# Kernel tuning notes

Hardware: AMD Instinct MI355X
Metric: run time of the kernel (lower is better)

The kernel has to match this reference:

```python
import jax, jax.numpy as jnp
import numpy as np

D_MODEL = 1024
N_HEADS = 16
HEAD_DIM = D_MODEL // N_HEADS


def setup_inputs() -> dict:
    key = jax.random.key(0)
    ks = jax.random.split(key, 9)
    s = 1.0 / np.sqrt(D_MODEL)
    mk = lambda k: jax.random.uniform(k, (D_MODEL, D_MODEL), jnp.float32, -s, s)
    mb = lambda k: jax.random.uniform(k, (D_MODEL,), jnp.float32, -s, s)
    return {
        "x": jax.random.normal(ks[0], (2, 2048, D_MODEL), jnp.float32),
        "Wq": mk(ks[1]), "bq": mb(ks[2]),
        "Wk": mk(ks[3]), "bk": mb(ks[4]),
        "Wv": mk(ks[5]), "bv": mb(ks[6]),
        "Wo": mk(ks[7]), "bo": mb(ks[8]),
    }


def _split_heads(t, B, S):
    # [B,S,D] -> [B,H,S,hd]
    return t.reshape(B, S, N_HEADS, HEAD_DIM).transpose(0, 2, 1, 3)


def reference(x, Wq, bq, Wk, bk, Wv, bv, Wo, bo):
    B, S, _ = x.shape
    # torch Linear: y = x @ W.T + b  (W stored [out, in])
    Q = _split_heads(x @ Wq.T + bq, B, S)
    K = _split_heads(x @ Wk.T + bk, B, S)
    V = _split_heads(x @ Wv.T + bv, B, S)
    scores = jnp.einsum("bhsd,bhtd->bhst", Q, K) / np.sqrt(HEAD_DIM).astype(np.float32)
    attn = jax.nn.softmax(scores, axis=-1)
    out = jnp.einsum("bhst,bhtd->bhsd", attn, V)
    out = out.transpose(0, 2, 1, 3).reshape(B, S, D_MODEL)
    return out @ Wo.T + bo
```

## Files before the change

kernel.cpp:

```cpp
#include <hip/hip_runtime.h>
#include <math.h>

#define D_MODEL 1024
#define NH 16
#define HD 64
#define SEQ 2048
#define NB 2
#define BSROWS (NB * SEQ)
#define NT (SEQ / 64)

typedef __attribute__((ext_vector_type(8)))  short short8;
typedef __attribute__((ext_vector_type(4)))  float f32x4;
typedef __attribute__((ext_vector_type(16))) float f32x16;

__device__ __forceinline__ ushort bf16rne(float f) {
    union { float f; uint32_t u; } v; v.f = f;
    return (ushort)((v.u + 0x7FFFu + ((v.u >> 16) & 1u)) >> 16);
}

__device__ __forceinline__ float hw_exp2(float x) {
    float r;
    asm("v_exp_f32 %0, %1" : "=v"(r) : "v"(x));
    return r;
}

__device__ __forceinline__ void permswap(uint32_t& a, uint32_t& b) {
    asm("v_permlane32_swap_b32 %0, %1" : "+v"(a), "+v"(b));
}

__device__ __forceinline__ void gl_lds16(const void* g, void* l) {
    __builtin_amdgcn_global_load_lds(
        reinterpret_cast<const uint32_t __attribute__((address_space(1)))*>(
            reinterpret_cast<uintptr_t>(g)),
        reinterpret_cast<uint32_t __attribute__((address_space(3)))*>(
            reinterpret_cast<uintptr_t>(l)),
        16, 0, 0);
}

__global__ __launch_bounds__(256) void convert_all(const float* __restrict__ x,
                                                   const float* __restrict__ w0,
                                                   const float* __restrict__ w1,
                                                   const float* __restrict__ w2,
                                                   const float* __restrict__ w3,
                                                   ushort* __restrict__ xb,
                                                   ushort* __restrict__ qkv,
                                                   ushort* __restrict__ wo) {
    const int which = blockIdx.y;
    const float* src;
    ushort* dst;
    int i;
    if (which < 4) {
        src = (which == 0) ? w0 : (which == 1) ? w1 : (which == 2) ? w2 : w3;
        dst = (which < 3) ? (qkv + (size_t)which * D_MODEL * D_MODEL) : wo;
        i   = blockIdx.x * 256 + threadIdx.x;
    } else {
        src = x;
        dst = xb;
        i   = ((which - 4) * 512 + blockIdx.x) * 256 + threadIdx.x;
    }
    const float4 a = ((const float4*)src)[2 * i];
    const float4 b = ((const float4*)src)[2 * i + 1];
    union { ushort u[8]; uint4 v; } r;
    r.u[0] = bf16rne(a.x); r.u[1] = bf16rne(a.y); r.u[2] = bf16rne(a.z); r.u[3] = bf16rne(a.w);
    r.u[4] = bf16rne(b.x); r.u[5] = bf16rne(b.y); r.u[6] = bf16rne(b.z); r.u[7] = bf16rne(b.w);
    ((uint4*)dst)[i] = r.v;
}

template <int BN, int MODE>
__global__ __launch_bounds__(256) void gemm_mfma(const ushort* __restrict__ A,
                                                 const ushort* __restrict__ B,
                                                 const float* __restrict__ b0,
                                                 const float* __restrict__ b1,
                                                 const float* __restrict__ b2,
                                                 void* __restrict__ o0v,
                                                 void* __restrict__ o1v,
                                                 void* __restrict__ o2v) {
    constexpr int BM = 128, BK = 32;
    constexpr int WN = (BN == 128) ? 64 : 32;
    constexpr int NM = 4;
    constexpr int NN = WN / 16;

    __shared__ ushort As[BM * BK];
    __shared__ ushort Bs[BN * BK];

    const int tid = threadIdx.x;
    const int w   = tid >> 6;
    const int l   = tid & 63;
    const int i0  = blockIdx.x * BM;
    const int n0  = blockIdx.y * BN;

    const int wr = (w >> 1) * 64;
    const int wc = (w & 1) * WN;

    const int srow = l >> 2;
    const int scol = (l & 3) * 8;
    const ushort* ga = A + (size_t)(i0 + w * 32 + srow) * D_MODEL + scol;
    const ushort* gb = B + (size_t)(n0 + w * (BN / 4) + srow) * D_MODEL + scol;
    ushort* lA = &As[(w * 32) * BK];
    ushort* lB = &Bs[(w * (BN / 4)) * BK];

    f32x4 acc[NM][NN];
#pragma unroll
    for (int m = 0; m < NM; ++m)
#pragma unroll
        for (int n = 0; n < NN; ++n) acc[m][n] = (f32x4){0.f, 0.f, 0.f, 0.f};

    const int fr = l & 15;
    const int kc = (l >> 4) * 8;

    for (int k0 = 0; k0 < D_MODEL; k0 += BK) {
        __syncthreads();
        gl_lds16(ga, lA);
        gl_lds16(ga + 16 * D_MODEL, lA + 16 * BK);
        gl_lds16(gb, lB);
        if (BN == 128) gl_lds16(gb + 16 * D_MODEL, lB + 16 * BK);
        ga += BK; gb += BK;
        __syncthreads();

        short8 af[NM], bfr[NN];
#pragma unroll
        for (int m = 0; m < NM; ++m)
            af[m] = *(const short8*)&As[(wr + m * 16 + fr) * BK + kc];
#pragma unroll
        for (int n = 0; n < NN; ++n)
            bfr[n] = *(const short8*)&Bs[(wc + n * 16 + fr) * BK + kc];
#pragma unroll
        for (int m = 0; m < NM; ++m)
#pragma unroll
            for (int n = 0; n < NN; ++n)
                acc[m][n] = __builtin_amdgcn_mfma_f32_16x16x32_bf16(af[m], bfr[n], acc[m][n], 0, 0, 0);
    }

    const int rr = (l >> 4) * 4;

    if (MODE == 1) {
        float* out = (float*)o0v;
#pragma unroll
        for (int n = 0; n < NN; ++n) {
            const int j = n0 + wc + n * 16 + fr;
            const float bj = b0[j];
#pragma unroll
            for (int m = 0; m < NM; ++m) {
                const int row = i0 + wr + m * 16 + rr;
#pragma unroll
                for (int r = 0; r < 4; ++r)
                    out[(size_t)(row + r) * D_MODEL + j] = acc[m][n][r] + bj;
            }
        }
    } else {
        const int p = n0 >> 10;
        const float* bias = (p == 0) ? b0 : (p == 1) ? b1 : b2;
        const float scl = (p == 0) ? 0.18033688011112042f : 1.0f;
#pragma unroll
        for (int n = 0; n < NN; ++n) {
            const int j = n0 + wc + n * 16 + fr;
            const int f = j & 1023;
            const float bj = bias[f];
            const int h = f >> 6, d = f & 63;
#pragma unroll
            for (int m = 0; m < NM; ++m) {
                const int row = i0 + wr + m * 16 + rr;
                const int bb = row >> 11;
                const int s0 = row & (SEQ - 1);
                if (p < 2) {
                    ushort* dst = (ushort*)(p == 0 ? o0v : o1v);
#pragma unroll
                    for (int r = 0; r < 4; ++r)
                        dst[(((size_t)bb * NH + h) * SEQ + (s0 + r)) * HD + d] =
                            bf16rne((acc[m][n][r] + bj) * scl);
                } else {
                    ushort4 pk;
                    pk.x = bf16rne(acc[m][n][0] + bj);
                    pk.y = bf16rne(acc[m][n][1] + bj);
                    pk.z = bf16rne(acc[m][n][2] + bj);
                    pk.w = bf16rne(acc[m][n][3] + bj);
                    *(ushort4*)&((ushort*)o2v)[(((size_t)bb * NH + h) * HD + d) * SEQ + s0] = pk;
                }
            }
        }
    }
}

__global__ __launch_bounds__(256) void attn_mfma9(const ushort* __restrict__ Q,
                                                  const ushort* __restrict__ K,
                                                  const ushort* __restrict__ Vt,
                                                  ushort* __restrict__ Aout) {
    __shared__ ushort KsB[2 * 4096];
    __shared__ ushort VtsB[2 * 4096];

    const int tid = threadIdx.x;
    const int w   = tid >> 6;
    const int l   = tid & 63;
    const int lq  = l & 31;
    const int hi  = l >> 5;
    const int id  = blockIdx.x;
    const int qt  = id >> 5;
    const int b   = (id >> 4) & 1;
    const int h   = id & 15;
    const size_t bh = (size_t)b * NH + h;

    const ushort* Qg = Q  + (bh * SEQ + (size_t)qt * 128 + w * 32 + lq) * HD;
    const ushort* Kg = K  + bh * SEQ * HD;
    const ushort* Vg = Vt + bh * HD * SEQ;

    short8 qf[4];
#pragma unroll
    for (int dk = 0; dk < 4; ++dk)
        qf[dk] = *(const short8*)&Qg[dk * 16 + hi * 8];

    int srow[2], scol[2], ssw[2];
#pragma unroll
    for (int j = 0; j < 2; ++j) {
        const int idx = tid + j * 256;
        srow[j] = idx >> 3;
        scol[j] = (idx & 7) * 8;
        ssw[j]  = scol[j] ^ ((srow[j] & 7) << 3);
    }

    uint4 kreg[2], vreg[2];
#pragma unroll
    for (int j = 0; j < 2; ++j) {
        kreg[j] = *(const uint4*)&Kg[(size_t)srow[j] * HD + scol[j]];
        vreg[j] = *(const uint4*)&Vg[(size_t)srow[j] * SEQ + scol[j]];
    }
#pragma unroll
    for (int j = 0; j < 2; ++j) {
        *(uint4*)&KsB [srow[j] * 64 + ssw[j]] = kreg[j];
        *(uint4*)&VtsB[srow[j] * 64 + ssw[j]] = vreg[j];
    }
    __syncthreads();

    f32x16 oa0a, oa0b, oa1a, oa1b;
#pragma unroll
    for (int r = 0; r < 16; ++r) { oa0a[r] = 0.f; oa0b[r] = 0.f; oa1a[r] = 0.f; oa1b[r] = 0.f; }
    float m = -3.0e38f, lsum = 0.f;

    for (int kt = 0; kt < NT; ++kt) {
        const ushort* Ks  = &KsB [(kt & 1) * 4096];
        const ushort* Vts = &VtsB[(kt & 1) * 4096];
        ushort* Ksn  = &KsB [((kt + 1) & 1) * 4096];
        ushort* Vtsn = &VtsB[((kt + 1) & 1) * 4096];

        if (kt + 1 < NT) {
#pragma unroll
            for (int j = 0; j < 2; ++j) {
                kreg[j] = *(const uint4*)&Kg[((size_t)(kt + 1) * 64 + srow[j]) * HD + scol[j]];
                vreg[j] = *(const uint4*)&Vg[(size_t)srow[j] * SEQ + (kt + 1) * 64 + scol[j]];
            }
        }

        f32x16 sc0, sc1;
#pragma unroll
        for (int r = 0; r < 16; ++r) { sc0[r] = 0.f; sc1[r] = 0.f; }
        const int ksw0 = (lq & 7) << 3;
        __builtin_amdgcn_s_setprio(1);
#pragma unroll
        for (int dk = 0; dk < 4; ++dk) {
            const int col = (dk * 16 + hi * 8) ^ ksw0;
            const short8 kf0 = *(const short8*)&Ks[lq * 64 + col];
            const short8 kf1 = *(const short8*)&Ks[(32 + lq) * 64 + col];
            sc0 = __builtin_amdgcn_mfma_f32_32x32x16_bf16(kf0, qf[dk], sc0, 0, 0, 0);
            sc1 = __builtin_amdgcn_mfma_f32_32x32x16_bf16(kf1, qf[dk], sc1, 0, 0, 0);
        }
        __builtin_amdgcn_s_setprio(0);

        float t0 = fmaxf(fmaxf(sc0[0], sc0[1]), fmaxf(sc0[2], sc0[3]));
        float t1 = fmaxf(fmaxf(sc0[4], sc0[5]), fmaxf(sc0[6], sc0[7]));
        float t2 = fmaxf(fmaxf(sc0[8], sc0[9]), fmaxf(sc0[10], sc0[11]));
        float t3 = fmaxf(fmaxf(sc0[12], sc0[13]), fmaxf(sc0[14], sc0[15]));
        float u0 = fmaxf(fmaxf(sc1[0], sc1[1]), fmaxf(sc1[2], sc1[3]));
        float u1 = fmaxf(fmaxf(sc1[4], sc1[5]), fmaxf(sc1[6], sc1[7]));
        float u2 = fmaxf(fmaxf(sc1[8], sc1[9]), fmaxf(sc1[10], sc1[11]));
        float u3 = fmaxf(fmaxf(sc1[12], sc1[13]), fmaxf(sc1[14], sc1[15]));
        float pm = fmaxf(fmaxf(fmaxf(t0, t1), fmaxf(t2, t3)),
                         fmaxf(fmaxf(u0, u1), fmaxf(u2, u3)));
        pm = fmaxf(pm, __shfl_xor(pm, 32));

        if (!__all(pm - m <= 11.0f)) {
            const float mn = fmaxf(m, pm);
            const float corr = hw_exp2(m - mn);
            m = mn; lsum *= corr;
#pragma unroll
            for (int r = 0; r < 16; ++r) {
                oa0a[r] *= corr; oa0b[r] *= corr;
                oa1a[r] *= corr; oa1b[r] *= corr;
            }
        }

        float p0[16], p1[16];
#pragma unroll
        for (int r = 0; r < 16; ++r) { p0[r] = hw_exp2(sc0[r] - m); p1[r] = hw_exp2(sc1[r] - m); }
        lsum += (((p0[0] + p0[1]) + (p0[2] + p0[3])) + ((p0[4] + p0[5]) + (p0[6] + p0[7])))
              + (((p0[8] + p0[9]) + (p0[10] + p0[11])) + ((p0[12] + p0[13]) + (p0[14] + p0[15])))
              + (((p1[0] + p1[1]) + (p1[2] + p1[3])) + ((p1[4] + p1[5]) + (p1[6] + p1[7])))
              + (((p1[8] + p1[9]) + (p1[10] + p1[11])) + ((p1[12] + p1[13]) + (p1[14] + p1[15])));

        uint32_t pk0[8], pk1[8];
#pragma unroll
        for (int i = 0; i < 8; ++i) {
            asm("v_cvt_pk_bf16_f32 %0, %1, %2" : "=v"(pk0[i]) : "v"(p0[2 * i]), "v"(p0[2 * i + 1]));
            asm("v_cvt_pk_bf16_f32 %0, %1, %2" : "=v"(pk1[i]) : "v"(p1[2 * i]), "v"(p1[2 * i + 1]));
        }
        permswap(pk0[0], pk0[2]); permswap(pk0[1], pk0[3]);
        permswap(pk0[4], pk0[6]); permswap(pk0[5], pk0[7]);
        permswap(pk1[0], pk1[2]); permswap(pk1[1], pk1[3]);
        permswap(pk1[4], pk1[6]); permswap(pk1[5], pk1[7]);

        union U8 { uint32_t u[4]; short8 s; };
        U8 f00, f01, f10, f11;
        f00.u[0] = pk0[0]; f00.u[1] = pk0[1]; f00.u[2] = pk0[2]; f00.u[3] = pk0[3];
        f01.u[0] = pk0[4]; f01.u[1] = pk0[5]; f01.u[2] = pk0[6]; f01.u[3] = pk0[7];
        f10.u[0] = pk1[0]; f10.u[1] = pk1[1]; f10.u[2] = pk1[2]; f10.u[3] = pk1[3];
        f11.u[0] = pk1[4]; f11.u[1] = pk1[5]; f11.u[2] = pk1[6]; f11.u[3] = pk1[7];
        const short8 pf00 = f00.s, pf01 = f01.s, pf10 = f10.s, pf11 = f11.s;

        const int d0 = lq, d1 = 32 + lq;
        const int vsw0 = (d0 & 7) << 3;
        const int tA = hi * 8;
        const short8 vA0 = *(const short8*)&Vts[d0 * 64 + ((tA)      ^ vsw0)];
        const short8 vA1 = *(const short8*)&Vts[d1 * 64 + ((tA)      ^ vsw0)];
        const short8 vB0 = *(const short8*)&Vts[d0 * 64 + ((tA + 16) ^ vsw0)];
        const short8 vB1 = *(const short8*)&Vts[d1 * 64 + ((tA + 16) ^ vsw0)];
        const short8 wA0 = *(const short8*)&Vts[d0 * 64 + ((tA + 32) ^ vsw0)];
        const short8 wA1 = *(const short8*)&Vts[d1 * 64 + ((tA + 32) ^ vsw0)];
        const short8 wB0 = *(const short8*)&Vts[d0 * 64 + ((tA + 48) ^ vsw0)];
        const short8 wB1 = *(const short8*)&Vts[d1 * 64 + ((tA + 48) ^ vsw0)];
        __builtin_amdgcn_s_setprio(1);
        oa0a = __builtin_amdgcn_mfma_f32_32x32x16_bf16(vA0, pf00, oa0a, 0, 0, 0);
        oa1a = __builtin_amdgcn_mfma_f32_32x32x16_bf16(vA1, pf00, oa1a, 0, 0, 0);
        oa0b = __builtin_amdgcn_mfma_f32_32x32x16_bf16(vB0, pf01, oa0b, 0, 0, 0);
        oa1b = __builtin_amdgcn_mfma_f32_32x32x16_bf16(vB1, pf01, oa1b, 0, 0, 0);
        oa0a = __builtin_amdgcn_mfma_f32_32x32x16_bf16(wA0, pf10, oa0a, 0, 0, 0);
        oa1a = __builtin_amdgcn_mfma_f32_32x32x16_bf16(wA1, pf10, oa1a, 0, 0, 0);
        oa0b = __builtin_amdgcn_mfma_f32_32x32x16_bf16(wB0, pf11, oa0b, 0, 0, 0);
        oa1b = __builtin_amdgcn_mfma_f32_32x32x16_bf16(wB1, pf11, oa1b, 0, 0, 0);
        __builtin_amdgcn_s_setprio(0);

        if (kt + 1 < NT) {
#pragma unroll
            for (int j = 0; j < 2; ++j) {
                *(uint4*)&Ksn [srow[j] * 64 + ssw[j]] = kreg[j];
                *(uint4*)&Vtsn[srow[j] * 64 + ssw[j]] = vreg[j];
            }
        }
        __syncthreads();
    }

    lsum += __shfl_xor(lsum, 32);
    const float inv = 1.f / lsum;

    f32x16 oa0, oa1;
#pragma unroll
    for (int r = 0; r < 16; ++r) {
        oa0[r] = oa0a[r] + oa0b[r];
        oa1[r] = oa1a[r] + oa1b[r];
    }

    ushort* Ow = KsB + w * 2048;
#pragma unroll
    for (int r = 0; r < 16; ++r) {
        const int dd = (r & 3) + 8 * (r >> 2) + 4 * hi;
        const int swq = (lq & 7) << 3;
        Ow[lq * 64 + ((dd)      ^ swq)] = bf16rne(oa0[r] * inv);
        Ow[lq * 64 + ((dd + 32) ^ swq)] = bf16rne(oa1[r] * inv);
    }
    const size_t orow0 = (size_t)b * SEQ + (size_t)qt * 128 + w * 32;
#pragma unroll
    for (int i = 0; i < 4; ++i) {
        const int row = (l >> 3) + 8 * i;
        const int d0 = (l & 7) * 8;
        const uint4 v = *(const uint4*)&Ow[row * 64 + (d0 ^ ((row & 7) << 3))];
        *(uint4*)&Aout[(orow0 + row) * D_MODEL + h * HD + d0] = v;
    }
}

extern "C" void kernel_launch(void* const* d_in, const int* in_sizes, int n_in,
                              void* d_out, int out_size, void* d_ws, size_t ws_size,
                              hipStream_t stream) {
    const float* x  = (const float*)d_in[0];
    const float* Wq = (const float*)d_in[1];
    const float* bq = (const float*)d_in[2];
    const float* Wk = (const float*)d_in[3];
    const float* bk = (const float*)d_in[4];
    const float* Wv = (const float*)d_in[5];
    const float* bv = (const float*)d_in[6];
    const float* Wo = (const float*)d_in[7];
    const float* bo = (const float*)d_in[8];
    float* out = (float*)d_out;

    ushort* xb   = (ushort*)d_ws;
    ushort* Wqkv = xb   + (size_t)BSROWS * D_MODEL;
    ushort* Wob  = Wqkv + (size_t)3 * D_MODEL * D_MODEL;
    ushort* Qw   = Wob  + (size_t)D_MODEL * D_MODEL;
    ushort* Kw   = Qw   + (size_t)BSROWS * D_MODEL;
    ushort* Vw   = Kw   + (size_t)BSROWS * D_MODEL;
    ushort* Ab   = Vw   + (size_t)BSROWS * D_MODEL;

    convert_all<<<dim3(512, 8), 256, 0, stream>>>(x, Wq, Wk, Wv, Wo, xb, Wqkv, Wob);

    gemm_mfma<128, 0><<<dim3(32, 24), 256, 0, stream>>>(
        xb, Wqkv, bq, bk, bv, Qw, Kw, Vw);

    attn_mfma9<<<dim3((SEQ / 128) * NH * NB), 256, 0, stream>>>(Qw, Kw, Vw, Ab);

    gemm_mfma<64, 1><<<dim3(32, 16), 256, 0, stream>>>(
        Ab, Wob, bo, nullptr, nullptr, out, nullptr, nullptr);
}
```

Before: 126.9 us.

## Triple-buffer K/V tiles and software-pipeline QK^T one tile ahead in attention

Moves the attention kernel from double to triple LDS buffering for K/V tiles. The global prefetch now runs two tiles ahead, and the QK^T MFMAs for tile kt+1 are issued before the softmax and PV work of tile kt, with one barrier per iteration at the top. The goal is to overlap matrix-core work with softmax VALU work and hide global load latency. In exchange, LDS use rises from 32KB to 48KB per block and extra score accumulators raise register pressure, which may reduce occupancy.

After: 191.8 us. 51.1% more time.

```diff
diff --git a/kernel.cpp b/kernel.cpp
--- a/kernel.cpp
+++ b/kernel.cpp
@@ -35,6 +35,24 @@
         reinterpret_cast<uint32_t __attribute__((address_space(3)))*>(
             reinterpret_cast<uintptr_t>(l)),
         16, 0, 0);
+}
+
+__device__ __forceinline__ void qkt32(const ushort* __restrict__ Ks,
+                                      int lq, int hi, const short8* qf,
+                                      f32x16& s0, f32x16& s1) {
+#pragma unroll
+    for (int r = 0; r < 16; ++r) { s0[r] = 0.f; s1[r] = 0.f; }
+    const int ksw0 = (lq & 7) << 3;
+    __builtin_amdgcn_s_setprio(1);
+#pragma unroll
+    for (int dk = 0; dk < 4; ++dk) {
+        const int col = (dk * 16 + hi * 8) ^ ksw0;
+        const short8 kf0 = *(const short8*)&Ks[lq * 64 + col];
+        const short8 kf1 = *(const short8*)&Ks[(32 + lq) * 64 + col];
+        s0 = __builtin_amdgcn_mfma_f32_32x32x16_bf16(kf0, qf[dk], s0, 0, 0, 0);
+        s1 = __builtin_amdgcn_mfma_f32_32x32x16_bf16(kf1, qf[dk], s1, 0, 0, 0);
+    }
+    __builtin_amdgcn_s_setprio(0);
 }
 
 __global__ __launch_bounds__(256) void convert_all(const float* __restrict__ x,
@@ -181,12 +199,12 @@
     }
 }
 
-__global__ __launch_bounds__(256) void attn_mfma9(const ushort* __restrict__ Q,
-                                                  const ushort* __restrict__ K,
-                                                  const ushort* __restrict__ Vt,
-                                                  ushort* __restrict__ Aout) {
-    __shared__ ushort KsB[2 * 4096];
-    __shared__ ushort VtsB[2 * 4096];
+__global__ __launch_bounds__(256) void attn_mfma10(const ushort* __restrict__ Q,
+                                                   const ushort* __restrict__ K,
+                                                   const ushort* __restrict__ Vt,
+                                                   ushort* __restrict__ Aout) {
+    __shared__ ushort KsB[3 * 4096];
+    __shared__ ushort VtsB[3 * 4096];
 
     const int tid = threadIdx.x;
     const int w   = tid >> 6;
@@ -219,50 +237,58 @@
 
     uint4 kreg[2], vreg[2];
 #pragma unroll
+    for (int t = 0; t < 2; ++t) {
+#pragma unroll
+        for (int j = 0; j < 2; ++j) {
+            kreg[j] = *(const uint4*)&Kg[((size_t)t * 64 + srow[j]) * HD + scol[j]];
+            vreg[j] = *(const uint4*)&Vg[(size_t)srow[j] * SEQ + t * 64 + scol[j]];
+        }
+#pragma unroll
+        for (int j = 0; j < 2; ++j) {
+            *(uint4*)&KsB [t * 4096 + srow[j] * 64 + ssw[j]] = kreg[j];
+            *(uint4*)&VtsB[t * 4096 + srow[j] * 64 + ssw[j]] = vreg[j];
+        }
+    }
+#pragma unroll
     for (int j = 0; j < 2; ++j) {
-        kreg[j] = *(const uint4*)&Kg[(size_t)srow[j] * HD + scol[j]];
-        vreg[j] = *(const uint4*)&Vg[(size_t)srow[j] * SEQ + scol[j]];
-    }
-#pragma unroll
-    for (int j = 0; j < 2; ++j) {
-        *(uint4*)&KsB [srow[j] * 64 + ssw[j]] = kreg[j];
-        *(uint4*)&VtsB[srow[j] * 64 + ssw[j]] = vreg[j];
+        kreg[j] = *(const uint4*)&Kg[((size_t)2 * 64 + srow[j]) * HD + scol[j]];
+        vreg[j] = *(const uint4*)&Vg[(size_t)srow[j] * SEQ + 2 * 64 + scol[j]];
     }
     __syncthreads();
+
+    f32x16 sc0, sc1;
+    qkt32(KsB, lq, hi, qf, sc0, sc1);
 
     f32x16 oa0a, oa0b, oa1a, oa1b;
 #pragma unroll
     for (int r = 0; r < 16; ++r) { oa0a[r] = 0.f; oa0b[r] = 0.f; oa1a[r] = 0.f; oa1b[r] = 0.f; }
     float m = -3.0e38f, lsum = 0.f;
 
+    int cur = 0, nxt = 1, wr3 = 2;
+
     for (int kt = 0; kt < NT; ++kt) {
-        const ushort* Ks  = &KsB [(kt & 1) * 4096];
-        const ushort* Vts = &VtsB[(kt & 1) * 4096];
-        ushort* Ksn  = &KsB [((kt + 1) & 1) * 4096];
-        ushort* Vtsn = &VtsB[((kt + 1) & 1) * 4096];
-
-        if (kt + 1 < NT) {
+        __syncthreads();
+
+        if (kt + 2 < NT) {
 #pragma unroll
             for (int j = 0; j < 2; ++j) {
-                kreg[j] = *(const uint4*)&Kg[((size_t)(kt + 1) * 64 + srow[j]) * HD + scol[j]];
-                vreg[j] = *(const uint4*)&Vg[(size_t)srow[j] * SEQ + (kt + 1) * 64 + scol[j]];
+                *(uint4*)&KsB [wr3 * 4096 + srow[j] * 64 + ssw[j]] = kreg[j];
+                *(uint4*)&VtsB[wr3 * 4096 + srow[j] * 64 + ssw[j]] = vreg[j];
             }
         }
-
-        f32x16 sc0, sc1;
-#pragma unroll
-        for (int r = 0; r < 16; ++r) { sc0[r] = 0.f; sc1[r] = 0.f; }
-        const int ksw0 = (lq & 7) << 3;
-        __builtin_amdgcn_s_setprio(1);
-#pragma unroll
-        for (int dk = 0; dk < 4; ++dk) {
-            const int col = (dk * 16 + hi * 8) ^ ksw0;
-            const short8 kf0 = *(const short8*)&Ks[lq * 64 + col];
-            const short8 kf1 = *(const short8*)&Ks[(32 + lq) * 64 + col];
-            sc0 = __builtin_amdgcn_mfma_f32_32x32x16_bf16(kf0, qf[dk], sc0, 0, 0, 0);
-            sc1 = __builtin_amdgcn_mfma_f32_32x32x16_bf16(kf1, qf[dk], sc1, 0, 0, 0);
-        }
-        __builtin_amdgcn_s_setprio(0);
+        if (kt + 3 < NT) {
+#pragma unroll
+            for (int j = 0; j < 2; ++j) {
+                kreg[j] = *(const uint4*)&Kg[((size_t)(kt + 3) * 64 + srow[j]) * HD + scol[j]];
+                vreg[j] = *(const uint4*)&Vg[(size_t)srow[j] * SEQ + (kt + 3) * 64 + scol[j]];
+            }
+        }
+
+        f32x16 sn0, sn1;
+#pragma unroll
+        for (int r = 0; r < 16; ++r) { sn0[r] = 0.f; sn1[r] = 0.f; }
+        const bool have_next = (kt + 1 < NT);
+        if (have_next) qkt32(KsB + nxt * 4096, lq, hi, qf, sn0, sn1);
 
         float t0 = fmaxf(fmaxf(sc0[0], sc0[1]), fmaxf(sc0[2], sc0[3]));
         float t1 = fmaxf(fmaxf(sc0[4], sc0[5]), fmaxf(sc0[6], sc0[7]));
@@ -314,6 +340,7 @@
         f11.u[0] = pk1[4]; f11.u[1] = pk1[5]; f11.u[2] = pk1[6]; f11.u[3] = pk1[7];
         const short8 pf00 = f00.s, pf01 = f01.s, pf10 = f10.s, pf11 = f11.s;
 
+        const ushort* Vts = VtsB + cur * 4096;
         const int d0 = lq, d1 = 32 + lq;
         const int vsw0 = (d0 & 7) << 3;
         const int tA = hi * 8;
@@ -336,14 +363,9 @@
         oa1b = __builtin_amdgcn_mfma_f32_32x32x16_bf16(wB1, pf11, oa1b, 0, 0, 0);
         __builtin_amdgcn_s_setprio(0);
 
-        if (kt + 1 < NT) {
-#pragma unroll
-            for (int j = 0; j < 2; ++j) {
-                *(uint4*)&Ksn [srow[j] * 64 + ssw[j]] = kreg[j];
-                *(uint4*)&Vtsn[srow[j] * 64 + ssw[j]] = vreg[j];
-            }
-        }
-        __syncthreads();
+        if (have_next) { sc0 = sn0; sc1 = sn1; }
+
+        const int t = cur; cur = nxt; nxt = wr3; wr3 = t;
     }
 
     lsum += __shfl_xor(lsum, 32);
@@ -401,7 +423,7 @@
     gemm_mfma<128, 0><<<dim3(32, 24), 256, 0, stream>>>(
         xb, Wqkv, bq, bk, bv, Qw, Kw, Vw);
 
-    attn_mfma9<<<dim3((SEQ / 128) * NH * NB), 256, 0, stream>>>(Qw, Kw, Vw, Ab);
+    attn_mfma10<<<dim3((SEQ / 128) * NH * NB), 256, 0, stream>>>(Qw, Kw, Vw, Ab);
 
     gemm_mfma<64, 1><<<dim3(32, 16), 256, 0, stream>>>(
         Ab, Wob, bo, nullptr, nullptr, out, nullptr, nullptr);
```
